# Optimization experiments

Measured on AMD Instinct MI355X. Metric: run time of the kernel, lower is better.

The kernel has to match this reference:

```python
import jax, jax.numpy as jnp
import numpy as np

NEG_SLOPE = 0.2  # PyG GATConv default leaky_relu slope


def gat_layer(x, W, a_src, a_dst, b):
    # x: [B, N, Fin]; W: [Fin, H*C]; a_src/a_dst: [H, C]; b: [H*C]
    # Dense-block equivalent of PyG GATConv on a fully-connected block graph
    # (self loops included), concat=True.
    B, N, Fin = x.shape
    H, C = a_src.shape
    h = jnp.einsum('bnf,fhc->bnhc', x, W.reshape(Fin, H, C))  # [B,N,H,C]
    ls = jnp.einsum('bnhc,hc->bnh', h, a_src)  # alpha_src per node
    ld = jnp.einsum('bnhc,hc->bnh', h, a_dst)  # alpha_dst per node
    # logits[i, j] = leaky_relu(alpha_dst[i] + alpha_src[j]); softmax over j
    logits = jax.nn.leaky_relu(ld[:, :, None, :] + ls[:, None, :, :], NEG_SLOPE)  # [B,i,j,H]
    attn = jax.nn.softmax(logits, axis=2)
    out = jnp.einsum('bijh,bjhc->bihc', attn, h).reshape(B, N, H * C)
    return out + b


def setup_inputs() -> dict:
    key = jax.random.key(0)
    ks = jax.random.split(key, 12)
    bs, R, Nc, enc = 8, 256, 64, 31
    H, hid, out = 8, 64, 32
    Fin = 1 + enc  # 32
    p = lambda k, shape: jax.random.normal(k, shape, jnp.float32) * 0.05
    return {
        'xs': jax.random.normal(ks[0], (bs, R, Nc), jnp.float32),
        'pos_enc': jax.random.normal(ks[1], (bs, Nc, enc), jnp.float32),
        'W1': p(ks[2], (Fin, H * hid)), 'as1': p(ks[3], (H, hid)), 'ad1': p(ks[4], (H, hid)),
        'b1': jnp.zeros((H * hid,), jnp.float32),
        'W2': p(ks[5], (H * hid, H * hid)), 'as2': p(ks[6], (H, hid)), 'ad2': p(ks[7], (H, hid)),
        'b2': jnp.zeros((H * hid,), jnp.float32),
        'W3': p(ks[8], (H * hid, H * out)), 'as3': p(ks[9], (H, out)), 'ad3': p(ks[10], (H, out)),
        'b3': jnp.zeros((H * out,), jnp.float32),
    }


def reference(xs, pos_enc, W1, as1, ad1, b1, W2, as2, ad2, b2, W3, as3, ad3, b3):
    bs, R, Nc = xs.shape
    enc = pos_enc.shape[-1]
    pe = jnp.broadcast_to(pos_enc[:, None], (bs, R, Nc, enc))
    x = jnp.concatenate([xs[..., None], pe], axis=-1)  # [bs,R,Nc,1+enc]
    x = x.reshape(bs * R, Nc, 1 + enc)  # independent fully-connected blocks
    x = gat_layer(x, W1, as1, ad1, b1)
    x = gat_layer(x, W2, as2, ad2, b2)
    x = gat_layer(x, W3, as3, ad3, b3)
    out = x.reshape(bs, R, Nc, -1).mean(axis=2)  # mean over num_xs
    return out
```

## Files before the change

### kernel.cpp

```cpp
#include <hip/hip_runtime.h>
#include <hip/hip_bf16.h>

typedef __hip_bfloat16 bf16;
typedef unsigned int uint32;
typedef __attribute__((ext_vector_type(8))) short short8;
typedef __attribute__((ext_vector_type(4))) float float4v;
typedef __attribute__((ext_vector_type(16))) float float16v;

#define THREADS 512
#define LDX 520
#define LDE 68
#define LOG2E 1.44269504088896340736f

__device__ __forceinline__ bf16 f2b(float x) { return __float2bfloat16(x); }
__device__ __forceinline__ uint32 packbf2(float x, float y) {
  union { __hip_bfloat162 b; uint32 u; } cv;
  cv.b = __float22bfloat162_rn(make_float2(x, y));
  return cv.u;
}
__device__ __forceinline__ bf16 f2b1(float x) {
  union { uint32 u; unsigned short s[2]; } cv;
  cv.u = packbf2(x, x);
  union { unsigned short s; bf16 b; } r;
  r.s = cv.s[0];
  return r.b;
}
__device__ __forceinline__ float exp2_hw(float x) {
#if __has_builtin(__builtin_amdgcn_exp2f)
  return __builtin_amdgcn_exp2f(x);
#else
  float r;
  asm("v_exp_f32 %0, %1" : "=v"(r) : "v"(x));
  return r;
#endif
}
__device__ __forceinline__ float rcp_hw(float x) {
#if __has_builtin(__builtin_amdgcn_rcpf)
  return __builtin_amdgcn_rcpf(x);
#else
  float r;
  asm("v_rcp_f32 %0, %1" : "=v"(r) : "v"(x));
  return r;
#endif
}
__device__ __forceinline__ void lane32_swap(uint32 a, uint32 b, int q,
                                            uint32& lo, uint32& hi) {
#if __has_builtin(__builtin_amdgcn_permlane32_swap)
  auto r = __builtin_amdgcn_permlane32_swap(a, b, false, false);
  lo = r[0];
  hi = r[1];
  (void)q;
#else
  uint32 pa = (uint32)__shfl_xor((int)a, 32, 64);
  uint32 pb = (uint32)__shfl_xor((int)b, 32, 64);
  lo = q ? pb : a;
  hi = q ? b : pa;
#endif
}

__global__ void prep_all(const float* __restrict__ W1, const float* __restrict__ W2,
                         const float* __restrict__ W3,
                         const float* __restrict__ as1, const float* __restrict__ ad1,
                         const float* __restrict__ as2, const float* __restrict__ ad2,
                         const float* __restrict__ as3, const float* __restrict__ ad3,
                         bf16* __restrict__ dst, bf16* __restrict__ dstE) {
  const int b = blockIdx.x;
  const int t = threadIdx.x;
  if (b < 1600) {
    int o = b * 256 + t;
    const float* W;
    int Mlog, loc, dbase;
    if (o < 16384) { W = W1; Mlog = 9; loc = o; dbase = 0; }
    else if (o < 278528) { W = W2; Mlog = 9; loc = o - 16384; dbase = 16384; }
    else { W = W3; Mlog = 8; loc = o - 278528; dbase = 278528; }
    float v = W[loc];
    int M = 1 << Mlog;
    int n = loc & (M - 1), k = loc >> Mlog;
    int kb = k >> 4, q = (k >> 3) & 1, j = k & 7;
    dst[dbase + ((kb * M + n) * 2 + q) * 8 + j] = f2b(v);
    return;
  }
  const int kr = (b - 1600) * 4 + (t >> 6);
  const int l = t & 63;
  const float *W, *as_, *ad_;
  int M, lk, dbase;
  if (kr < 32)       { W = W1; as_ = as1; ad_ = ad1; M = 512; lk = kr;       dbase = 0; }
  else if (kr < 544) { W = W2; as_ = as2; ad_ = ad2; M = 512; lk = kr - 32;  dbase = 512; }
  else               { W = W3; as_ = as3; ad_ = ad3; M = 256; lk = kr - 544; dbase = 8704; }
  const float* wr = W + (size_t)lk * M;
  float ps = 0.f, pd = 0.f;
  if (M == 512) {
    float4 w0 = *(const float4*)(wr + 8 * l);
    float4 w1 = *(const float4*)(wr + 8 * l + 4);
    float4 s0 = *(const float4*)(as_ + 8 * l);
    float4 s1 = *(const float4*)(as_ + 8 * l + 4);
    float4 d0 = *(const float4*)(ad_ + 8 * l);
    float4 d1 = *(const float4*)(ad_ + 8 * l + 4);
    ps = w0.x * s0.x + w0.y * s0.y + w0.z * s0.z + w0.w * s0.w +
         w1.x * s1.x + w1.y * s1.y + w1.z * s1.z + w1.w * s1.w;
    pd = w0.x * d0.x + w0.y * d0.y + w0.z * d0.z + w0.w * d0.w +
         w1.x * d1.x + w1.y * d1.y + w1.z * d1.z + w1.w * d1.w;
  } else {
    float4 w0 = *(const float4*)(wr + 4 * l);
    float4 s0 = *(const float4*)(as_ + 4 * l);
    float4 d0 = *(const float4*)(ad_ + 4 * l);
    ps = w0.x * s0.x + w0.y * s0.y + w0.z * s0.z + w0.w * s0.w;
    pd = w0.x * d0.x + w0.y * d0.y + w0.z * d0.z + w0.w * d0.w;
  }
#pragma unroll
  for (int m = 1; m < 8; m <<= 1) {
    ps += __shfl_xor(ps, m, 64);
    pd += __shfl_xor(pd, m, 64);
  }
  const int j = lk & 7, kc = (lk >> 3) & 3, ks = lk >> 5;
  const int h = l >> 3;
  const int base = dbase + ks * 512 + kc * 8 + j;
  if ((l & 7) == 0) dstE[base + h * 32] = f2b(ps * LOG2E);
  if ((l & 7) == 1) dstE[base + (8 + h) * 32] = f2b(pd * LOG2E);
}

template <int K, int M, int C, bool LAST>
__device__ __forceinline__ void gat_layer(
    int t, const bf16* __restrict__ Wswz, const bf16* __restrict__ WE,
    const float* __restrict__ bias, bf16* sX, float* sE) {
  constexpr int NCT = C / 32;
  constexpr int KS16 = K / 16;
  constexpr int KSE = K / 32;
  const int lane = t & 63;
  const int hu = __builtin_amdgcn_readfirstlane(t >> 6);
  const int c = lane & 31, q = lane >> 5;
  const int ln16 = lane & 15, kq16 = lane >> 4;
  const int colbase = hu * C;

  if (hu < 4) {
    float4v acce = (float4v)0.f;
    float4v acce2 = (float4v)0.f;
#pragma unroll
    for (int ks = 0; ks < KSE; ks += 2) {
      short8 afrE = *(const short8*)(sX + (hu * 16 + ln16) * LDX + ks * 32 + kq16 * 8);
      short8 efr = *(const short8*)(WE + ks * 512 + ln16 * 32 + kq16 * 8);
      acce = __builtin_amdgcn_mfma_f32_16x16x32_bf16(afrE, efr, acce, 0, 0, 0);
      if constexpr (KSE > 1) {
        short8 afrE2 = *(const short8*)(sX + (hu * 16 + ln16) * LDX + (ks + 1) * 32 + kq16 * 8);
        short8 efr2 = *(const short8*)(WE + (ks + 1) * 512 + ln16 * 32 + kq16 * 8);
        acce2 = __builtin_amdgcn_mfma_f32_16x16x32_bf16(afrE2, efr2, acce2, 0, 0, 0);
      }
    }
    if constexpr (KSE > 1) acce = acce + acce2;
    *(float4v*)(sE + ln16 * LDE + hu * 16 + kq16 * 4) = acce;
  }
  __syncthreads();

  uint32 Ppk[NCT][4][4];
  {
    float16v acc[2][NCT];
#pragma unroll
    for (int rt = 0; rt < 2; ++rt)
#pragma unroll
      for (int ct = 0; ct < NCT; ++ct) acc[rt][ct] = (float16v)0.f;
    const bf16* ap = sX + c * LDX + q * 8;
    const bf16* bp = Wswz + ((colbase + c) * 2 + q) * 8;
#pragma unroll 8
    for (int ks = 0; ks < KS16; ++ks) {
      short8 afr[2];
      afr[0] = *(const short8*)(ap + ks * 16);
      afr[1] = *(const short8*)(ap + 32 * LDX + ks * 16);
      short8 bfr[NCT];
#pragma unroll
      for (int ct = 0; ct < NCT; ++ct)
        bfr[ct] = *(const short8*)(bp + (size_t)ks * (M * 16) + ct * 32 * 16);
#pragma unroll
      for (int rt = 0; rt < 2; ++rt)
#pragma unroll
        for (int ct = 0; ct < NCT; ++ct)
          acc[rt][ct] = __builtin_amdgcn_mfma_f32_32x32x16_bf16(
              afr[rt], bfr[ct], acc[rt][ct], 0, 0, 0);
    }
#pragma unroll
    for (int rt = 0; rt < 2; ++rt)
#pragma unroll
      for (int ct = 0; ct < NCT; ++ct)
#pragma unroll
        for (int tp = 0; tp < 2; ++tp) {
          Ppk[ct][rt * 2 + tp][0] = packbf2(acc[rt][ct][8 * tp + 0], acc[rt][ct][8 * tp + 1]);
          Ppk[ct][rt * 2 + tp][1] = packbf2(acc[rt][ct][8 * tp + 2], acc[rt][ct][8 * tp + 3]);
          Ppk[ct][rt * 2 + tp][2] = packbf2(acc[rt][ct][8 * tp + 4], acc[rt][ct][8 * tp + 5]);
          Ppk[ct][rt * 2 + tp][3] = packbf2(acc[rt][ct][8 * tp + 6], acc[rt][ct][8 * tp + 7]);
        }
  }

  const float* lsrow = sE + hu * LDE;
  const float* ldrow = sE + (8 + hu) * LDE;
  short8 pfr[2][4];
#pragma unroll
  for (int rt = 0; rt < 2; ++rt) {
    const float ldi = ldrow[rt * 32 + c];
    float pe_[4][8];
    float rs[4];
#pragma unroll
    for (int tt = 0; tt < 4; ++tt) {
      float4 v0 = *(const float4*)(lsrow + tt * 16 + q * 8);
      float4 v1 = *(const float4*)(lsrow + tt * 16 + q * 8 + 4);
      float ls8[8] = {v0.x, v0.y, v0.z, v0.w, v1.x, v1.y, v1.z, v1.w};
      float s = 0.f;
#pragma unroll
      for (int jj = 0; jj < 8; ++jj) {
        float tv = ldi + ls8[jj];
        float e = exp2_hw(fmaxf(tv, 0.2f * tv));
        pe_[tt][jj] = e;
        s += e;
      }
      rs[tt] = s;
    }
    float rsum = (rs[0] + rs[1]) + (rs[2] + rs[3]);
    rsum += __shfl_xor(rsum, 32, 64);
    const float ri = rcp_hw(rsum);
#pragma unroll
    for (int tt = 0; tt < 4; ++tt) {
      union { uint32 d[4]; short8 s; } w;
#pragma unroll
      for (int jp = 0; jp < 4; ++jp)
        w.d[jp] = packbf2(pe_[tt][2 * jp] * ri, pe_[tt][2 * jp + 1] * ri);
      pfr[rt][tt] = w.s;
    }
  }

  __syncthreads();

#pragma unroll
  for (int ct = 0; ct < NCT; ++ct) {
    short8 hfr[4];
#pragma unroll
    for (int tt = 0; tt < 4; ++tt) {
      uint32 U0 = Ppk[ct][tt][0], U1 = Ppk[ct][tt][1];
      uint32 V0 = Ppk[ct][tt][2], V1 = Ppk[ct][tt][3];
      uint32 d0, d1, d2, d3;
      lane32_swap(U0, V0, q, d0, d2);
      lane32_swap(U1, V1, q, d1, d3);
      union { uint32 d[4]; short8 s; } u;
      u.d[0] = d0; u.d[1] = d1; u.d[2] = d2; u.d[3] = d3;
      hfr[tt] = u.s;
    }
    float16v oacc[2];
    oacc[0] = (float16v)0.f;
    oacc[1] = (float16v)0.f;
#pragma unroll
    for (int tt = 0; tt < 4; ++tt) {
      oacc[0] = __builtin_amdgcn_mfma_f32_32x32x16_bf16(pfr[0][tt], hfr[tt], oacc[0], 0, 0, 0);
      oacc[1] = __builtin_amdgcn_mfma_f32_32x32x16_bf16(pfr[1][tt], hfr[tt], oacc[1], 0, 0, 0);
    }
    const float bv = bias[colbase + ct * 32 + c];
#pragma unroll
    for (int rt = 0; rt < 2; ++rt)
#pragma unroll
      for (int r = 0; r < 16; ++r) {
        float val = oacc[rt][r] + bv;
        int row = rt * 32 + (r & 3) + 8 * (r >> 2) + 4 * q;
        if constexpr (LAST)
          ((float*)sX)[row * 260 + colbase + ct * 32 + c] = val;
        else
          sX[row * LDX + colbase + ct * 32 + c] = f2b1(val);
      }
  }
  __syncthreads();
}

__global__ __launch_bounds__(THREADS, 4) void gat3_mfma(
    const float* __restrict__ xs, const float* __restrict__ pe,
    const bf16* __restrict__ W1s, const bf16* __restrict__ WE1,
    const float* __restrict__ b1, const bf16* __restrict__ W2s,
    const bf16* __restrict__ WE2, const float* __restrict__ b2,
    const bf16* __restrict__ W3s, const bf16* __restrict__ WE3,
    const float* __restrict__ b3, float* __restrict__ out) {
  extern __shared__ char smem[];
  bf16* sX = (bf16*)smem;
  float* sE = (float*)(smem + 66560);

  const int t = threadIdx.x;
  const int blk = blockIdx.x;
  const int bidx = blk >> 8;

  for (int idx = t; idx < 64 * 32; idx += THREADS) {
    int n = idx >> 5, f = idx & 31;
    float v = (f == 0) ? xs[blk * 64 + n] : pe[(bidx * 64 + n) * 31 + (f - 1)];
    sX[n * LDX + f] = f2b(v);
  }
  __syncthreads();

  gat_layer<32, 512, 64, false>(t, W1s, WE1, b1, sX, sE);
  gat_layer<512, 512, 64, false>(t, W2s, WE2, b2, sX, sE);
  gat_layer<512, 256, 32, true>(t, W3s, WE3, b3, sX, sE);

  const float* xf = (const float*)sX;
  if (t < 256) {
    float s = 0.f;
#pragma unroll 8
    for (int i = 0; i < 64; ++i) s += xf[i * 260 + t];
    out[blk * 256 + t] = s * 0.015625f;
  }
}

extern "C" void kernel_launch(void* const* d_in, const int* in_sizes, int n_in,
                              void* d_out, int out_size, void* d_ws, size_t ws_size,
                              hipStream_t stream) {
  const float* xs = (const float*)d_in[0];
  const float* pe = (const float*)d_in[1];
  const float* W1 = (const float*)d_in[2];
  const float* as1 = (const float*)d_in[3];
  const float* ad1 = (const float*)d_in[4];
  const float* b1 = (const float*)d_in[5];
  const float* W2 = (const float*)d_in[6];
  const float* as2 = (const float*)d_in[7];
  const float* ad2 = (const float*)d_in[8];
  const float* b2 = (const float*)d_in[9];
  const float* W3 = (const float*)d_in[10];
  const float* as3 = (const float*)d_in[11];
  const float* ad3 = (const float*)d_in[12];
  const float* b3 = (const float*)d_in[13];

  bf16* Wall = (bf16*)d_ws;
  bf16* WEall = Wall + 409600;
  bf16* W1s = Wall;
  bf16* W2s = Wall + 16384;
  bf16* W3s = Wall + 278528;
  bf16* WE1 = WEall;
  bf16* WE2 = WEall + 512;
  bf16* WE3 = WEall + 8704;

  prep_all<<<dim3(1864), dim3(256), 0, stream>>>(
      W1, W2, W3, as1, ad1, as2, ad2, as3, ad3, Wall, WEall);

  static bool smem_inited = false;
  if (!smem_inited) {
    (void)hipFuncSetAttribute((const void*)gat3_mfma,
                              hipFuncAttributeMaxDynamicSharedMemorySize,
                              70912);
    smem_inited = true;
  }
  gat3_mfma<<<dim3(2048), dim3(THREADS), 70912, stream>>>(
      xs, pe, W1s, WE1, b1, W2s, WE2, b2, W3s, WE3, b3, (float*)d_out);
}
```

Baseline: 236.9 us.

## Process two graph blocks per workgroup with a staggered layer-phase pipeline

The main kernel now launches 1024-thread workgroups that each handle two graph blocks, using double-buffered shared feature and logit arrays. The two 512-thread groups are offset by one phase: one runs the projection GEMM while the other runs softmax and the attention-times-features product. The aim is to overlap MFMA-heavy and exp-heavy work and to cut the number of barriers per layer. The lane swap of the projected features moves into the projection phase so the result can be held in registers across a barrier. The weight-prep kernel also switches to float4 loads, so each thread converts four weights. The risks are the larger shared-memory footprint (about 139 KB per workgroup) and register pressure under launch_bounds(1024,4), which may limit residency or cause spills.

```diff
diff --git a/kernel.cpp b/kernel.cpp
--- a/kernel.cpp
+++ b/kernel.cpp
@@ -7,7 +7,7 @@
 typedef __attribute__((ext_vector_type(4))) float float4v;
 typedef __attribute__((ext_vector_type(16))) float float16v;
 
-#define THREADS 512
+#define THREADS 1024
 #define LDX 520
 #define LDE 68
 #define LOG2E 1.44269504088896340736f
@@ -66,21 +66,25 @@
                          bf16* __restrict__ dst, bf16* __restrict__ dstE) {
   const int b = blockIdx.x;
   const int t = threadIdx.x;
-  if (b < 1600) {
-    int o = b * 256 + t;
+  if (b < 400) {
+    int o = (b * 256 + t) * 4;
     const float* W;
     int Mlog, loc, dbase;
     if (o < 16384) { W = W1; Mlog = 9; loc = o; dbase = 0; }
     else if (o < 278528) { W = W2; Mlog = 9; loc = o - 16384; dbase = 16384; }
     else { W = W3; Mlog = 8; loc = o - 278528; dbase = 278528; }
-    float v = W[loc];
+    float4 v = *(const float4*)(W + loc);
     int M = 1 << Mlog;
     int n = loc & (M - 1), k = loc >> Mlog;
     int kb = k >> 4, q = (k >> 3) & 1, j = k & 7;
-    dst[dbase + ((kb * M + n) * 2 + q) * 8 + j] = f2b(v);
+    int base = dbase + ((kb * M + n) * 2 + q) * 8 + j;
+    dst[base] = f2b(v.x);
+    dst[base + 16] = f2b(v.y);
+    dst[base + 32] = f2b(v.z);
+    dst[base + 48] = f2b(v.w);
     return;
   }
-  const int kr = (b - 1600) * 4 + (t >> 6);
+  const int kr = (b - 400) * 4 + (t >> 6);
   const int l = t & 63;
   const float *W, *as_, *ad_;
   int M, lk, dbase;
@@ -119,19 +123,12 @@
   if ((l & 7) == 1) dstE[base + (8 + h) * 32] = f2b(pd * LOG2E);
 }
 
-template <int K, int M, int C, bool LAST>
-__device__ __forceinline__ void gat_layer(
-    int t, const bf16* __restrict__ Wswz, const bf16* __restrict__ WE,
-    const float* __restrict__ bias, bf16* sX, float* sE) {
-  constexpr int NCT = C / 32;
-  constexpr int KS16 = K / 16;
+
+template <int K>
+__device__ __forceinline__ void phaseE(int lane, int hu, const bf16* __restrict__ WE,
+                                       const bf16* sX, float* sE) {
   constexpr int KSE = K / 32;
-  const int lane = t & 63;
-  const int hu = __builtin_amdgcn_readfirstlane(t >> 6);
-  const int c = lane & 31, q = lane >> 5;
   const int ln16 = lane & 15, kq16 = lane >> 4;
-  const int colbase = hu * C;
-
   if (hu < 4) {
     float4v acce = (float4v)0.f;
     float4v acce2 = (float4v)0.f;
@@ -149,46 +146,63 @@
     if constexpr (KSE > 1) acce = acce + acce2;
     *(float4v*)(sE + ln16 * LDE + hu * 16 + kq16 * 4) = acce;
   }
-  __syncthreads();
-
-  uint32 Ppk[NCT][4][4];
-  {
-    float16v acc[2][NCT];
+}
+
+template <int K, int M, int C>
+__device__ __forceinline__ void phaseP1(int lane, int hu, const bf16* __restrict__ Wswz,
+                                        const bf16* sX, uint32 (&PB)[2][4][4]) {
+  constexpr int NCT = C / 32, KS16 = K / 16;
+  const int c = lane & 31, q = lane >> 5;
+  const int colbase = hu * C;
+  float16v acc[2][NCT];
+#pragma unroll
+  for (int rt = 0; rt < 2; ++rt)
+#pragma unroll
+    for (int ct = 0; ct < NCT; ++ct) acc[rt][ct] = (float16v)0.f;
+  const bf16* ap = sX + c * LDX + q * 8;
+  const bf16* bp = Wswz + ((colbase + c) * 2 + q) * 8;
+#pragma unroll 4
+  for (int ks = 0; ks < KS16; ++ks) {
+    short8 afr[2];
+    afr[0] = *(const short8*)(ap + ks * 16);
+    afr[1] = *(const short8*)(ap + 32 * LDX + ks * 16);
+    short8 bfr[NCT];
+#pragma unroll
+    for (int ct = 0; ct < NCT; ++ct)
+      bfr[ct] = *(const short8*)(bp + (size_t)ks * (M * 16) + ct * 32 * 16);
 #pragma unroll
     for (int rt = 0; rt < 2; ++rt)
 #pragma unroll
-      for (int ct = 0; ct < NCT; ++ct) acc[rt][ct] = (float16v)0.f;
-    const bf16* ap = sX + c * LDX + q * 8;
-    const bf16* bp = Wswz + ((colbase + c) * 2 + q) * 8;
-#pragma unroll 8
-    for (int ks = 0; ks < KS16; ++ks) {
-      short8 afr[2];
-      afr[0] = *(const short8*)(ap + ks * 16);
-      afr[1] = *(const short8*)(ap + 32 * LDX + ks * 16);
-      short8 bfr[NCT];
-#pragma unroll
       for (int ct = 0; ct < NCT; ++ct)
-        bfr[ct] = *(const short8*)(bp + (size_t)ks * (M * 16) + ct * 32 * 16);
-#pragma unroll
-      for (int rt = 0; rt < 2; ++rt)
-#pragma unroll
-        for (int ct = 0; ct < NCT; ++ct)
-          acc[rt][ct] = __builtin_amdgcn_mfma_f32_32x32x16_bf16(
-              afr[rt], bfr[ct], acc[rt][ct], 0, 0, 0);
-    }
+        acc[rt][ct] = __builtin_amdgcn_mfma_f32_32x32x16_bf16(
+            afr[rt], bfr[ct], acc[rt][ct], 0, 0, 0);
+  }
+#pragma unroll
+  for (int ct = 0; ct < NCT; ++ct)
 #pragma unroll
     for (int rt = 0; rt < 2; ++rt)
 #pragma unroll
-      for (int ct = 0; ct < NCT; ++ct)
-#pragma unroll
-        for (int tp = 0; tp < 2; ++tp) {
-          Ppk[ct][rt * 2 + tp][0] = packbf2(acc[rt][ct][8 * tp + 0], acc[rt][ct][8 * tp + 1]);
-          Ppk[ct][rt * 2 + tp][1] = packbf2(acc[rt][ct][8 * tp + 2], acc[rt][ct][8 * tp + 3]);
-          Ppk[ct][rt * 2 + tp][2] = packbf2(acc[rt][ct][8 * tp + 4], acc[rt][ct][8 * tp + 5]);
-          Ppk[ct][rt * 2 + tp][3] = packbf2(acc[rt][ct][8 * tp + 6], acc[rt][ct][8 * tp + 7]);
-        }
-  }
-
+      for (int tp = 0; tp < 2; ++tp) {
+        const int tt = rt * 2 + tp;
+        uint32 U0 = packbf2(acc[rt][ct][8 * tp + 0], acc[rt][ct][8 * tp + 1]);
+        uint32 U1 = packbf2(acc[rt][ct][8 * tp + 2], acc[rt][ct][8 * tp + 3]);
+        uint32 V0 = packbf2(acc[rt][ct][8 * tp + 4], acc[rt][ct][8 * tp + 5]);
+        uint32 V1 = packbf2(acc[rt][ct][8 * tp + 6], acc[rt][ct][8 * tp + 7]);
+        uint32 d0, d1, d2, d3;
+        lane32_swap(U0, V0, q, d0, d2);
+        lane32_swap(U1, V1, q, d1, d3);
+        PB[ct][tt][0] = d0; PB[ct][tt][1] = d1;
+        PB[ct][tt][2] = d2; PB[ct][tt][3] = d3;
+      }
+}
+
+template <int C, bool LAST>
+__device__ __forceinline__ void phaseSMPV(int lane, int hu, const float* __restrict__ bias,
+                                          bf16* sX, const float* sE,
+                                          const uint32 (&PB)[2][4][4]) {
+  constexpr int NCT = C / 32;
+  const int c = lane & 31, q = lane >> 5;
+  const int colbase = hu * C;
   const float* lsrow = sE + hu * LDE;
   const float* ldrow = sE + (8 + hu) * LDE;
   short8 pfr[2][4];
@@ -224,30 +238,18 @@
       pfr[rt][tt] = w.s;
     }
   }
-
-  __syncthreads();
-
 #pragma unroll
   for (int ct = 0; ct < NCT; ++ct) {
-    short8 hfr[4];
-#pragma unroll
-    for (int tt = 0; tt < 4; ++tt) {
-      uint32 U0 = Ppk[ct][tt][0], U1 = Ppk[ct][tt][1];
-      uint32 V0 = Ppk[ct][tt][2], V1 = Ppk[ct][tt][3];
-      uint32 d0, d1, d2, d3;
-      lane32_swap(U0, V0, q, d0, d2);
-      lane32_swap(U1, V1, q, d1, d3);
-      union { uint32 d[4]; short8 s; } u;
-      u.d[0] = d0; u.d[1] = d1; u.d[2] = d2; u.d[3] = d3;
-      hfr[tt] = u.s;
-    }
     float16v oacc[2];
     oacc[0] = (float16v)0.f;
     oacc[1] = (float16v)0.f;
 #pragma unroll
     for (int tt = 0; tt < 4; ++tt) {
-      oacc[0] = __builtin_amdgcn_mfma_f32_32x32x16_bf16(pfr[0][tt], hfr[tt], oacc[0], 0, 0, 0);
-      oacc[1] = __builtin_amdgcn_mfma_f32_32x32x16_bf16(pfr[1][tt], hfr[tt], oacc[1], 0, 0, 0);
+      union { uint32 d[4]; short8 s; } u;
+      u.d[0] = PB[ct][tt][0]; u.d[1] = PB[ct][tt][1];
+      u.d[2] = PB[ct][tt][2]; u.d[3] = PB[ct][tt][3];
+      oacc[0] = __builtin_amdgcn_mfma_f32_32x32x16_bf16(pfr[0][tt], u.s, oacc[0], 0, 0, 0);
+      oacc[1] = __builtin_amdgcn_mfma_f32_32x32x16_bf16(pfr[1][tt], u.s, oacc[1], 0, 0, 0);
     }
     const float bv = bias[colbase + ct * 32 + c];
 #pragma unroll
@@ -262,10 +264,9 @@
           sX[row * LDX + colbase + ct * 32 + c] = f2b1(val);
       }
   }
-  __syncthreads();
-}
-
-__global__ __launch_bounds__(THREADS, 4) void gat3_mfma(
+}
+
+__global__ __launch_bounds__(THREADS, 4) void gat3_pipe(
     const float* __restrict__ xs, const float* __restrict__ pe,
     const bf16* __restrict__ W1s, const bf16* __restrict__ WE1,
     const float* __restrict__ b1, const bf16* __restrict__ W2s,
@@ -273,30 +274,67 @@
     const bf16* __restrict__ W3s, const bf16* __restrict__ WE3,
     const float* __restrict__ b3, float* __restrict__ out) {
   extern __shared__ char smem[];
-  bf16* sX = (bf16*)smem;
-  float* sE = (float*)(smem + 66560);
+  bf16* sXA = (bf16*)smem;
+  bf16* sXB = (bf16*)(smem + 66560);
+  float* sEA = (float*)(smem + 133120);
+  float* sEB = (float*)(smem + 137472);
 
   const int t = threadIdx.x;
-  const int blk = blockIdx.x;
-  const int bidx = blk >> 8;
-
-  for (int idx = t; idx < 64 * 32; idx += THREADS) {
-    int n = idx >> 5, f = idx & 31;
-    float v = (f == 0) ? xs[blk * 64 + n] : pe[(bidx * 64 + n) * 31 + (f - 1)];
-    sX[n * LDX + f] = f2b(v);
+  const int lane = t & 63;
+  const int w = t >> 6;
+  const int G = w >> 3;
+  const int hu = __builtin_amdgcn_readfirstlane(w & 7);
+  const int blk0 = blockIdx.x * 2;
+
+  for (int idx = t; idx < 2 * 64 * 32; idx += THREADS) {
+    int g = idx >> 11, loc = idx & 2047;
+    int n = loc >> 5, f = loc & 31;
+    int blk = blk0 + g;
+    float v = (f == 0) ? xs[blk * 64 + n] : pe[((blk >> 8) * 64 + n) * 31 + (f - 1)];
+    (g ? sXB : sXA)[n * LDX + f] = f2b(v);
   }
   __syncthreads();
 
-  gat_layer<32, 512, 64, false>(t, W1s, WE1, b1, sX, sE);
-  gat_layer<512, 512, 64, false>(t, W2s, WE2, b2, sX, sE);
-  gat_layer<512, 256, 32, true>(t, W3s, WE3, b3, sX, sE);
-
-  const float* xf = (const float*)sX;
+  bf16* sXg = G ? sXB : sXA;
+  float* sEg = G ? sEB : sEA;
+
+  uint32 PB[2][4][4];
+#pragma unroll 1
+  for (int r = 0; r < 7; ++r) {
+    const int role = r + 1 - G;
+    if (role == 1) {
+      phaseE<32>(lane, hu, WE1, sXg, sEg);
+      phaseP1<32, 512, 64>(lane, hu, W1s, sXg, PB);
+    } else if (role == 2) {
+      phaseSMPV<64, false>(lane, hu, b1, sXg, sEg, PB);
+    } else if (role == 3) {
+      phaseE<512>(lane, hu, WE2, sXg, sEg);
+      phaseP1<512, 512, 64>(lane, hu, W2s, sXg, PB);
+    } else if (role == 4) {
+      phaseSMPV<64, false>(lane, hu, b2, sXg, sEg, PB);
+    } else if (role == 5) {
+      phaseE<512>(lane, hu, WE3, sXg, sEg);
+      phaseP1<512, 256, 32>(lane, hu, W3s, sXg, PB);
+    } else if (role == 6) {
+      phaseSMPV<32, true>(lane, hu, b3, sXg, sEg, PB);
+    } else if (role == 7) {
+      if (t < 256) {
+        const float* xf = (const float*)sXA;
+        float s = 0.f;
+#pragma unroll 8
+        for (int i = 0; i < 64; ++i) s += xf[i * 260 + t];
+        out[blk0 * 256 + t] = s * 0.015625f;
+      }
+    }
+    __syncthreads();
+  }
+
   if (t < 256) {
+    const float* xf = (const float*)sXB;
     float s = 0.f;
 #pragma unroll 8
     for (int i = 0; i < 64; ++i) s += xf[i * 260 + t];
-    out[blk * 256 + t] = s * 0.015625f;
+    out[(blk0 + 1) * 256 + t] = s * 0.015625f;
   }
 }
 
@@ -327,16 +365,16 @@
   bf16* WE2 = WEall + 512;
   bf16* WE3 = WEall + 8704;
 
-  prep_all<<<dim3(1864), dim3(256), 0, stream>>>(
+  prep_all<<<dim3(664), dim3(256), 0, stream>>>(
       W1, W2, W3, as1, ad1, as2, ad2, as3, ad3, Wall, WEall);
 
   static bool smem_inited = false;
   if (!smem_inited) {
-    (void)hipFuncSetAttribute((const void*)gat3_mfma,
+    (void)hipFuncSetAttribute((const void*)gat3_pipe,
                               hipFuncAttributeMaxDynamicSharedMemorySize,
-                              70912);
+                              141824);
     smem_inited = true;
   }
-  gat3_mfma<<<dim3(2048), dim3(THREADS), 70912, stream>>>(
+  gat3_pipe<<<dim3(1024), dim3(THREADS), 141824, stream>>>(
       xs, pe, W1s, WE1, b1, W2s, WE2, b2, W3s, WE3, b3, (float*)d_out);
 }
```

New measurement: 383.8 us. 62.0% more time.
